# Kernel tuning notes

Hardware: AMD Instinct MI355X
Metric: run time of the kernel (lower is better)

Reference implementation:

```python
import jax, jax.numpy as jnp
import numpy as np

N_NODES = 50000
N_EDGES = 800000
IN_CH, HID_CH, OUT_CH = 128, 128, 64


def _gcn_conv(x, W, b, src, dst, n):
    """PyG GCNConv: self-loops + symmetric norm + linear + scatter-add + bias."""
    loop = jnp.arange(n, dtype=src.dtype)
    src_sl = jnp.concatenate([src, loop])  # [E+N]
    dst_sl = jnp.concatenate([dst, loop])
    # degree computed on edges incl. self-loops (edge weight 1)
    deg = jax.ops.segment_sum(jnp.ones_like(dst_sl, dtype=x.dtype), dst_sl,
                              num_segments=n)
    dinv = jnp.where(deg > 0, jax.lax.rsqrt(deg), 0.0)
    norm = dinv[src_sl] * dinv[dst_sl]  # [E+N]
    xw = x @ W  # [N, F_out]
    msg = xw[src_sl] * norm[:, None]  # gather + scale, [E+N, F_out]
    out = jax.ops.segment_sum(msg, dst_sl, num_segments=n)
    return out + b


def setup_inputs() -> dict:
    key = jax.random.key(0)
    ks = jax.random.split(key, 5)
    x = jax.random.normal(ks[0], (N_NODES, IN_CH), dtype=jnp.float32)
    edge_index = jax.random.randint(ks[1], (2, N_EDGES), 0, N_NODES, dtype=jnp.int64)
    s1 = 1.0 / np.sqrt(IN_CH)
    s2 = 1.0 / np.sqrt(HID_CH)
    W1 = jax.random.normal(ks[2], (IN_CH, HID_CH), dtype=jnp.float32) * s1
    W2 = jax.random.normal(ks[3], (HID_CH, HID_CH), dtype=jnp.float32) * s2
    W3 = jax.random.normal(ks[4], (HID_CH, OUT_CH), dtype=jnp.float32) * s2
    return {
        "x": x, "edge_index": edge_index,
        "W1": W1, "b1": jnp.zeros((HID_CH,), jnp.float32),
        "W2": W2, "b2": jnp.zeros((HID_CH,), jnp.float32),
        "W3": W3, "b3": jnp.zeros((OUT_CH,), jnp.float32),
    }


def reference(x, edge_index, W1, b1, W2, b2, W3, b3):
    n = x.shape[0]
    src, dst = edge_index[0], edge_index[1]
    # dropout(p=0.6) is identity in eval mode
    h = jax.nn.relu(_gcn_conv(x, W1, b1, src, dst, n))
    h = jax.nn.relu(_gcn_conv(h, W2, b2, src, dst, n))
    out = _gcn_conv(h, W3, b3, src, dst, n)
    return out
```

## Files before the change

### kernel.cpp

```cpp
#include <hip/hip_runtime.h>
#include <cstdint>

#define CAP 32768
#define CHUNK 2048

typedef __attribute__((ext_vector_type(8))) short bf8_t;
typedef __attribute__((ext_vector_type(4))) float f4_t;

__device__ __forceinline__ uint32_t f_to_bf(float f) {
    union { float f; uint32_t u; } v; v.f = f;
    uint32_t u = v.u;
    return (u + 0x7fffu + ((u >> 16) & 1u)) >> 16;
}
__device__ __forceinline__ float bf_to_f(uint32_t h) {
    union { uint32_t u; float f; } v; v.u = h << 16; return v.f;
}
__device__ __forceinline__ float2 bf2_to_f2(uint32_t u) {
    union { uint32_t u; float f; } a, b;
    a.u = u << 16; b.u = u & 0xffff0000u;
    float2 r; r.x = a.f; r.y = b.f; return r;
}
__device__ __forceinline__ void fma8(float* acc, uint4 u, float d) {
    float2 p0 = bf2_to_f2(u.x), p1 = bf2_to_f2(u.y);
    float2 p2 = bf2_to_f2(u.z), p3 = bf2_to_f2(u.w);
    acc[0] += p0.x * d; acc[1] += p0.y * d;
    acc[2] += p1.x * d; acc[3] += p1.y * d;
    acc[4] += p2.x * d; acc[5] += p2.y * d;
    acc[6] += p3.x * d; acc[7] += p3.y * d;
}

__device__ __forceinline__ int detect64(const int* __restrict__ e32) {
    return (e32[1] | e32[3] | e32[5] | e32[7]) == 0;
}
__device__ __forceinline__ int edge_at(const void* edges, int is64, int idx) {
    if (is64) return (int)((const long long*)edges)[idx];
    return ((const int*)edges)[idx];
}

__global__ __launch_bounds__(256) void prep_kernel(
    const float* __restrict__ W1, const float* __restrict__ W2,
    const float* __restrict__ W3,
    uint16_t* w1h, uint16_t* w1l, uint16_t* w2h, uint16_t* w2l,
    uint16_t* w3h, uint16_t* w3l, int* __restrict__ bucket_cur) {
    if (blockIdx.x == 160) {
        if (threadIdx.x < 64) bucket_cur[threadIdx.x] = threadIdx.x * CAP;
        return;
    }
    int idx = blockIdx.x * 256 + threadIdx.x;
    const float* W; uint16_t* oh; uint16_t* ol; int FOUT; int e;
    if (idx < 16384)      { W = W1; oh = w1h; ol = w1l; FOUT = 128; e = idx; }
    else if (idx < 32768) { W = W2; oh = w2h; ol = w2l; FOUT = 128; e = idx - 16384; }
    else                  { W = W3; oh = w3h; ol = w3l; FOUT = 64;  e = idx - 32768; }
    int j = e & 7;
    int lane = (e >> 3) & 63;
    int rem = e >> 9;
    int NT = FOUT >> 4;
    int nt = rem % NT, kc = rem / NT;
    int k = kc * 32 + ((lane >> 4) << 3) + j;
    int c = nt * 16 + (lane & 15);
    float v = W[(size_t)k * FOUT + c];
    uint32_t h = f_to_bf(v);
    uint32_t l = f_to_bf(v - bf_to_f(h));
    oh[e] = (uint16_t)h;
    ol[e] = (uint16_t)l;
}

__device__ __forceinline__ void gemm1_body(
    const float* __restrict__ A, const uint16_t* __restrict__ Wfhi,
    const uint16_t* __restrict__ Wflo, uint16_t* __restrict__ Yout,
    int n, int cp, int tile0, int tstride, int lane) {
    constexpr int NT = 8, NTW = 2;
    int ntiles = (n + 15) >> 4;
    bf8_t wh[NTW][4], wl[NTW][4];
#pragma unroll
    for (int t = 0; t < NTW; t++) {
        int nt = cp * NTW + t;
#pragma unroll
        for (int kc = 0; kc < 4; kc++) {
            size_t b = ((size_t)(kc * NT + nt) * 64 + lane) * 8;
            wh[t][kc] = *(const bf8_t*)&Wfhi[b];
            wl[t][kc] = *(const bf8_t*)&Wflo[b];
        }
    }
    int row_in = lane & 15;
    int koff = (lane >> 4) << 3;
    int colb = lane & 15;
    int rq = (lane >> 4) << 2;
    for (int tile = tile0; tile < ntiles; tile += tstride) {
        int R = tile << 4;
        int arow = R + row_in; if (arow >= n) arow = n - 1;
        const float* ap = A + (size_t)arow * 128 + koff;
        bf8_t ah[4], al[4];
#pragma unroll
        for (int kc = 0; kc < 4; kc++) {
            float4 pv = *(const float4*)(ap + kc * 32);
            float4 qv = *(const float4*)(ap + kc * 32 + 4);
            float vv[8] = {pv.x, pv.y, pv.z, pv.w, qv.x, qv.y, qv.z, qv.w};
#pragma unroll
            for (int j = 0; j < 8; j++) {
                uint32_t h = f_to_bf(vv[j]);
                ah[kc][j] = (short)h;
                al[kc][j] = (short)f_to_bf(vv[j] - bf_to_f(h));
            }
        }
        f4_t acc[NTW];
#pragma unroll
        for (int t = 0; t < NTW; t++) acc[t] = (f4_t){0.f, 0.f, 0.f, 0.f};
#pragma unroll
        for (int kc = 0; kc < 4; kc++) {
#pragma unroll
            for (int t = 0; t < NTW; t++) {
                acc[t] = __builtin_amdgcn_mfma_f32_16x16x32_bf16(ah[kc], wh[t][kc], acc[t], 0, 0, 0);
                acc[t] = __builtin_amdgcn_mfma_f32_16x16x32_bf16(ah[kc], wl[t][kc], acc[t], 0, 0, 0);
                acc[t] = __builtin_amdgcn_mfma_f32_16x16x32_bf16(al[kc], wh[t][kc], acc[t], 0, 0, 0);
            }
        }
#pragma unroll
        for (int t = 0; t < NTW; t++) {
            int c = (cp * NTW + t) * 16 + colb;
#pragma unroll
            for (int r = 0; r < 4; r++) {
                int row = R + rq + r;
                if (row < n)
                    Yout[(size_t)row * 128 + c] = (uint16_t)f_to_bf(acc[t][r]);
            }
        }
    }
}

__global__ __launch_bounds__(256) void scatter_gemm1_kernel(
    const void* __restrict__ ei, int* __restrict__ bucket_cur,
    int2* __restrict__ buckets, int E, int sbcnt,
    const float* __restrict__ x, const uint16_t* __restrict__ w1h,
    const uint16_t* __restrict__ w1l, uint16_t* __restrict__ y1, int n) {
    int tid = threadIdx.x;
    if ((int)blockIdx.x < sbcnt) {
        __shared__ int cnt[64];
        int base = blockIdx.x * CHUNK;
        int is64 = detect64((const int*)ei);
        if (tid < 64) cnt[tid] = 0;
        __syncthreads();
        int dloc[8];
#pragma unroll
        for (int it = 0; it < 8; it++) {
            int i = base + it * 256 + tid;
            int d = (i < E) ? edge_at(ei, is64, E + i) : -1;
            dloc[it] = d;
            if (d >= 0) atomicAdd(&cnt[d >> 10], 1);
        }
        __syncthreads();
        if (tid < 64) {
            int v = cnt[tid];
            cnt[tid] = atomicAdd(&bucket_cur[tid], v);
        }
        __syncthreads();
#pragma unroll
        for (int it = 0; it < 8; it++) {
            int i = base + it * 256 + tid;
            if (dloc[it] >= 0) {
                int s = edge_at(ei, is64, i);
                int p = atomicAdd(&cnt[dloc[it] >> 10], 1);
                buckets[p] = make_int2(s, dloc[it]);
            }
        }
    } else {
        int lane = tid & 63, wid = tid >> 6;
        gemm1_body(x, w1h, w1l, y1, n, wid, blockIdx.x - sbcnt,
                   gridDim.x - sbcnt, lane);
    }
}

__global__ __launch_bounds__(512) void csr_local_kernel(
    const int2* __restrict__ buckets, const int* __restrict__ bucket_cur,
    int* __restrict__ row_ptr, int* __restrict__ bsum, float* __restrict__ dinv, int n) {
    __shared__ int cnt[1024];
    __shared__ int sb[1024];
    int b = blockIdx.x, tid = threadIdx.x;
    int base = b << 10;
    int lim = min(1024, n - base);
    if (lim <= 0) { if (tid == 0) bsum[b] = 0; return; }
    int ecnt = bucket_cur[b] - b * CAP;
    const int2* ebase = buckets + (size_t)b * CAP;
    for (int i = tid; i < 1024; i += 512) cnt[i] = 0;
    __syncthreads();
    for (int i = tid; i < ecnt; i += 512)
        atomicAdd(&cnt[ebase[i].y - base], 1);
    __syncthreads();
    for (int i = tid; i < lim; i += 512)
        dinv[base + i] = rsqrtf((float)(cnt[i] + 1));
    __syncthreads();
    int* a = cnt; int* s = sb;
    for (int st = 1; st < 1024; st <<= 1) {
        for (int i = tid; i < 1024; i += 512)
            s[i] = a[i] + ((i >= st) ? a[i - st] : 0);
        __syncthreads();
        int* t = a; a = s; s = t;
    }
    for (int i = tid; i < lim; i += 512)
        row_ptr[base + i] = (i > 0) ? a[i - 1] : 0;
    if (tid == 0) bsum[b] = a[1023];
}

__global__ __launch_bounds__(512) void fill_bucket_kernel(
    const int2* __restrict__ buckets, const int* __restrict__ bucket_cur,
    int* __restrict__ row_ptr, const int* __restrict__ bsum,
    int* __restrict__ col, int n, int nbuck) {
    __shared__ int cur[1024];
    __shared__ int s_bo;
    int b = blockIdx.x, tid = threadIdx.x;
    int base = b << 10;
    int lim = min(1024, n - base);
    if (lim <= 0) return;
    if (tid < 64) {
        int lane = tid;
        int v = (lane < nbuck) ? bsum[lane] : 0;
        int incl = v;
#pragma unroll
        for (int off = 1; off < 64; off <<= 1) {
            int t = __shfl_up(incl, off);
            if (lane >= off) incl += t;
        }
        int tot = __shfl(incl, nbuck - 1);
        int bo = (b > 0) ? __shfl(incl, b - 1) : 0;
        if (lane == 0) {
            s_bo = bo;
            if (b == nbuck - 1) row_ptr[n] = tot;
        }
    }
    __syncthreads();
    int ecnt = bucket_cur[b] - b * CAP;
    const int2* ebase = buckets + (size_t)b * CAP;
    int bo = s_bo;
    for (int i = tid; i < lim; i += 512) {
        int v = row_ptr[base + i] + bo;
        row_ptr[base + i] = v;
        cur[i] = v;
    }
    __syncthreads();
    for (int i = tid; i < ecnt; i += 512) {
        int2 e = ebase[i];
        int p = atomicAdd(&cur[e.y - base], 1);
        col[p] = e.x;
    }
}

template <int FOUT, bool SRC_SCALE>
__global__ __launch_bounds__(256) void agg_gemm_kernel(
    const uint16_t* __restrict__ Yin, const int* __restrict__ row_ptr,
    const int* __restrict__ col, const float* __restrict__ dinv,
    const float* __restrict__ bias,
    const uint16_t* __restrict__ Wfhi, const uint16_t* __restrict__ Wflo,
    uint16_t* __restrict__ Yout, int n) {
    __shared__ uint4 hs4[16 * 17];
    __shared__ uint4 ls4[16 * 17];
    int tid = threadIdx.x, wid = tid >> 6, lane = tid & 63;
    int base = blockIdx.x * 16;
    int g = lane & 15, j = lane >> 4;
    const uint4* Y4 = (const uint4*)Yin;

    float4 bb0 = *(const float4*)&bias[g * 8];
    float4 bb1 = *(const float4*)&bias[g * 8 + 4];
    float bb[8] = {bb0.x, bb0.y, bb0.z, bb0.w, bb1.x, bb1.y, bb1.z, bb1.w};

    for (int q = 0; q < 4; q++) {
        int r = wid * 4 + q, node = base + r;
        uint4 ph = (uint4){0, 0, 0, 0}, pl = (uint4){0, 0, 0, 0};
        if (node < n) {
            float di = dinv[node];
            float aA[8] = {}, aB[8] = {};
            {
                float sd = (j == 0) ? (SRC_SCALE ? di : 1.f) : 0.f;
                uint4 su = Y4[(size_t)node * 16 + g];
                fma8(aA, su, sd);
            }
            int start = row_ptr[node], end = row_ptr[node + 1];
            for (int b = start; b < end; b += 64) {
                int cnt = min(64, end - b);
                int sv = (b + lane < end) ? col[b + lane] : 0;
                for (int k = 0; k < cnt; k += 8) {
                    int iA = k + j, iB = k + 4 + j;
                    int sA = __shfl(sv, iA & 63);
                    int sB = __shfl(sv, iB & 63);
                    float dA = (iA < cnt) ? (SRC_SCALE ? dinv[sA] : 1.f) : 0.f;
                    float dB = (iB < cnt) ? (SRC_SCALE ? dinv[sB] : 1.f) : 0.f;
                    uint4 uA = Y4[(size_t)sA * 16 + g];
                    uint4 uB = Y4[(size_t)sB * 16 + g];
                    fma8(aA, uA, dA);
                    fma8(aB, uB, dB);
                }
            }
            float o[8];
#pragma unroll
            for (int t = 0; t < 8; t++) o[t] = aA[t] + aB[t];
#pragma unroll
            for (int t = 0; t < 8; t++) o[t] += __shfl_xor(o[t], 16);
#pragma unroll
            for (int t = 0; t < 8; t++) o[t] += __shfl_xor(o[t], 32);
            uint32_t hh[8];
#pragma unroll
            for (int t = 0; t < 8; t++) {
                o[t] = fmaxf(o[t] * di + bb[t], 0.f);
                hh[t] = f_to_bf(o[t]);
            }
            ph = (uint4){hh[0] | (hh[1] << 16), hh[2] | (hh[3] << 16),
                         hh[4] | (hh[5] << 16), hh[6] | (hh[7] << 16)};
            uint32_t ll[8];
#pragma unroll
            for (int t = 0; t < 8; t++) ll[t] = f_to_bf(o[t] - bf_to_f(hh[t]));
            pl = (uint4){ll[0] | (ll[1] << 16), ll[2] | (ll[3] << 16),
                         ll[4] | (ll[5] << 16), ll[6] | (ll[7] << 16)};
        }
        if (j == 0) {
            hs4[r * 17 + g] = ph;
            ls4[r * 17 + g] = pl;
        }
    }
    __syncthreads();

    const uint16_t* hs = (const uint16_t*)hs4;
    const uint16_t* ls = (const uint16_t*)ls4;
    constexpr int NT = FOUT / 16;
    constexpr int NTW = NT / 4;
    constexpr int LDW = 136;
    int cp = wid;
    bf8_t wh[NTW][4], wl[NTW][4];
#pragma unroll
    for (int t = 0; t < NTW; t++) {
        int nt = cp * NTW + t;
#pragma unroll
        for (int kc = 0; kc < 4; kc++) {
            size_t b = ((size_t)(kc * NT + nt) * 64 + lane) * 8;
            wh[t][kc] = *(const bf8_t*)&Wfhi[b];
            wl[t][kc] = *(const bf8_t*)&Wflo[b];
        }
    }
    int koff = (lane >> 4) << 3;
    int colb = lane & 15;
    int rq = (lane >> 4) << 2;
    bf8_t ah[4], al[4];
#pragma unroll
    for (int kc = 0; kc < 4; kc++) {
        ah[kc] = *(const bf8_t*)(hs + (lane & 15) * LDW + koff + kc * 32);
        al[kc] = *(const bf8_t*)(ls + (lane & 15) * LDW + koff + kc * 32);
    }
    f4_t acc[NTW];
#pragma unroll
    for (int t = 0; t < NTW; t++) acc[t] = (f4_t){0.f, 0.f, 0.f, 0.f};
#pragma unroll
    for (int kc = 0; kc < 4; kc++) {
#pragma unroll
        for (int t = 0; t < NTW; t++) {
            acc[t] = __builtin_amdgcn_mfma_f32_16x16x32_bf16(ah[kc], wh[t][kc], acc[t], 0, 0, 0);
            acc[t] = __builtin_amdgcn_mfma_f32_16x16x32_bf16(ah[kc], wl[t][kc], acc[t], 0, 0, 0);
            acc[t] = __builtin_amdgcn_mfma_f32_16x16x32_bf16(al[kc], wh[t][kc], acc[t], 0, 0, 0);
        }
    }
#pragma unroll
    for (int t = 0; t < NTW; t++) {
        int c = (cp * NTW + t) * 16 + colb;
#pragma unroll
        for (int r = 0; r < 4; r++) {
            int row = base + rq + r;
            if (row < n) {
                float v = acc[t][r] * dinv[row];
                Yout[(size_t)row * FOUT + c] = (uint16_t)f_to_bf(v);
            }
        }
    }
}

__global__ __launch_bounds__(256) void agg_final_kernel(
    const uint16_t* __restrict__ Y, const int* __restrict__ row_ptr,
    const int* __restrict__ col, const float* __restrict__ dinv,
    const float* __restrict__ bias, float* __restrict__ out, int n) {
    int w = blockIdx.x * 4 + (threadIdx.x >> 6);
    int lane = threadIdx.x & 63;
    if (w >= n) return;
    int g = lane & 7, j = lane >> 3;
    const uint4* Y4 = (const uint4*)Y;
    float4 bb0 = *(const float4*)&bias[g * 8];
    float4 bb1 = *(const float4*)&bias[g * 8 + 4];
    float bb[8] = {bb0.x, bb0.y, bb0.z, bb0.w, bb1.x, bb1.y, bb1.z, bb1.w};

    float aA[8] = {}, aB[8] = {};
    {
        uint4 su = Y4[(size_t)w * 8 + g];
        fma8(aA, su, (j == 0) ? 1.f : 0.f);
    }
    int start = row_ptr[w], end = row_ptr[w + 1];
    for (int b = start; b < end; b += 64) {
        int cnt = min(64, end - b);
        int sv = (b + lane < end) ? col[b + lane] : 0;
        for (int k = 0; k < cnt; k += 16) {
            int iA = k + j, iB = k + 8 + j;
            int sA = __shfl(sv, iA & 63);
            int sB = __shfl(sv, iB & 63);
            float dA = (iA < cnt) ? 1.f : 0.f;
            float dB = (iB < cnt) ? 1.f : 0.f;
            uint4 uA = Y4[(size_t)sA * 8 + g];
            uint4 uB = Y4[(size_t)sB * 8 + g];
            fma8(aA, uA, dA);
            fma8(aB, uB, dB);
        }
    }
    float o[8];
#pragma unroll
    for (int t = 0; t < 8; t++) o[t] = aA[t] + aB[t];
#pragma unroll
    for (int t = 0; t < 8; t++) o[t] += __shfl_xor(o[t], 8);
#pragma unroll
    for (int t = 0; t < 8; t++) o[t] += __shfl_xor(o[t], 16);
#pragma unroll
    for (int t = 0; t < 8; t++) o[t] += __shfl_xor(o[t], 32);
    float di = dinv[w];
#pragma unroll
    for (int t = 0; t < 8; t++) o[t] = o[t] * di + bb[t];
    if (j == 0) {
        float4 o0 = {o[0], o[1], o[2], o[3]};
        float4 o1 = {o[4], o[5], o[6], o[7]};
        *(float4*)&out[(size_t)w * 64 + g * 8] = o0;
        *(float4*)&out[(size_t)w * 64 + g * 8 + 4] = o1;
    }
}

extern "C" void kernel_launch(void* const* d_in, const int* in_sizes, int n_in,
                              void* d_out, int out_size, void* d_ws, size_t ws_size,
                              hipStream_t stream) {
    const float* x  = (const float*)d_in[0];
    const void*  ei = d_in[1];
    const float* W1 = (const float*)d_in[2];
    const float* b1 = (const float*)d_in[3];
    const float* W2 = (const float*)d_in[4];
    const float* b2 = (const float*)d_in[5];
    const float* W3 = (const float*)d_in[6];
    const float* b3 = (const float*)d_in[7];
    int n = in_sizes[0] / 128;
    int E = in_sizes[1] / 2;
    int nbuck = (n + 1023) >> 10;

    char* p = (char*)d_ws;
    auto carve = [&](size_t bytes) {
        char* r = p;
        p += (bytes + 255) & ~(size_t)255;
        return r;
    };
    float*    dinv       = (float*)carve((size_t)n * 4);
    int*      row_ptr    = (int*)carve((size_t)(n + 1) * 4);
    int*      bsum       = (int*)carve(64 * 4);
    int*      bucket_cur = (int*)carve(64 * 4);
    int*      col        = (int*)carve((size_t)E * 4);
    int2*     buckets    = (int2*)carve((size_t)64 * CAP * 8);
    uint16_t* y1         = (uint16_t*)carve((size_t)n * 128 * 2);
    uint16_t* y2         = (uint16_t*)carve((size_t)n * 128 * 2);
    uint16_t* y3         = (uint16_t*)carve((size_t)n * 64 * 2);
    uint16_t* w1h        = (uint16_t*)carve(128 * 128 * 2);
    uint16_t* w1l        = (uint16_t*)carve(128 * 128 * 2);
    uint16_t* w2h        = (uint16_t*)carve(128 * 128 * 2);
    uint16_t* w2l        = (uint16_t*)carve(128 * 128 * 2);
    uint16_t* w3h        = (uint16_t*)carve(128 * 64 * 2);
    uint16_t* w3l        = (uint16_t*)carve(128 * 64 * 2);

    int sbcnt = (E + CHUNK - 1) / CHUNK;
    int fb = (n + 15) / 16;

    prep_kernel<<<161, 256, 0, stream>>>(W1, W2, W3, w1h, w1l, w2h, w2l,
                                         w3h, w3l, bucket_cur);
    scatter_gemm1_kernel<<<sbcnt + 782, 256, 0, stream>>>(
        ei, bucket_cur, buckets, E, sbcnt, x, w1h, w1l, y1, n);
    csr_local_kernel<<<nbuck, 512, 0, stream>>>(buckets, bucket_cur, row_ptr, bsum, dinv, n);
    fill_bucket_kernel<<<nbuck, 512, 0, stream>>>(buckets, bucket_cur, row_ptr, bsum,
                                                  col, n, nbuck);
    agg_gemm_kernel<128, true><<<fb, 256, 0, stream>>>(
        y1, row_ptr, col, dinv, b1, w2h, w2l, y2, n);
    agg_gemm_kernel<64, false><<<fb, 256, 0, stream>>>(
        y2, row_ptr, col, dinv, b2, w3h, w3l, y3, n);
    agg_final_kernel<<<(n + 3) / 4, 256, 0, stream>>>(
        y3, row_ptr, col, dinv, b3, (float*)d_out, n);
}
```

Before: 243.0 us.

## Merge CSR build kernels and co-schedule weight prep and GEMM1 with graph stages

Restructures the launch plan: weight hi/lo splitting now runs in spare blocks of the edge-bucketing kernel, and the per-bucket count, scan and fill steps are merged into one kernel whose spare blocks run the first GEMM. Bucket counters are zeroed with a memset and used as per-bucket counts, so each block finds its offset by scanning those counts directly, which removes the separate bsum pass. This cuts kernel launches and the serial dependency chain, but the merged CSR kernel now runs each bucket with 256 threads instead of 512, and GEMM1 now waits on the scatter stage.

```diff
diff --git a/kernel.cpp b/kernel.cpp
--- a/kernel.cpp
+++ b/kernel.cpp
@@ -37,16 +37,11 @@
     return ((const int*)edges)[idx];
 }
 
-__global__ __launch_bounds__(256) void prep_kernel(
-    const float* __restrict__ W1, const float* __restrict__ W2,
+__device__ __forceinline__ void wsplit_body(
+    int idx, const float* __restrict__ W1, const float* __restrict__ W2,
     const float* __restrict__ W3,
     uint16_t* w1h, uint16_t* w1l, uint16_t* w2h, uint16_t* w2l,
-    uint16_t* w3h, uint16_t* w3l, int* __restrict__ bucket_cur) {
-    if (blockIdx.x == 160) {
-        if (threadIdx.x < 64) bucket_cur[threadIdx.x] = threadIdx.x * CAP;
-        return;
-    }
-    int idx = blockIdx.x * 256 + threadIdx.x;
+    uint16_t* w3h, uint16_t* w3l) {
     const float* W; uint16_t* oh; uint16_t* ol; int FOUT; int e;
     if (idx < 16384)      { W = W1; oh = w1h; ol = w1l; FOUT = 128; e = idx; }
     else if (idx < 32768) { W = W2; oh = w2h; ol = w2l; FOUT = 128; e = idx - 16384; }
@@ -65,6 +60,50 @@
     ol[e] = (uint16_t)l;
 }
 
+__global__ __launch_bounds__(256) void scatter_wprep_kernel(
+    const void* __restrict__ ei, int* __restrict__ bucket_cur,
+    int2* __restrict__ buckets, int E, int sbcnt,
+    const float* __restrict__ W1, const float* __restrict__ W2,
+    const float* __restrict__ W3,
+    uint16_t* w1h, uint16_t* w1l, uint16_t* w2h, uint16_t* w2l,
+    uint16_t* w3h, uint16_t* w3l) {
+    int tid = threadIdx.x;
+    if ((int)blockIdx.x >= sbcnt) {
+        int idx = (blockIdx.x - sbcnt) * 256 + tid;
+        wsplit_body(idx, W1, W2, W3, w1h, w1l, w2h, w2l, w3h, w3l);
+        return;
+    }
+    __shared__ int cnt[64];
+    int base = blockIdx.x * CHUNK;
+    int is64 = detect64((const int*)ei);
+    if (tid < 64) cnt[tid] = 0;
+    __syncthreads();
+    int dloc[8];
+#pragma unroll
+    for (int it = 0; it < 8; it++) {
+        int i = base + it * 256 + tid;
+        int d = (i < E) ? edge_at(ei, is64, E + i) : -1;
+        dloc[it] = d;
+        if (d >= 0) atomicAdd(&cnt[d >> 10], 1);
+    }
+    __syncthreads();
+    if (tid < 64) {
+        int v = cnt[tid];
+        cnt[tid] = atomicAdd(&bucket_cur[tid], v);
+    }
+    __syncthreads();
+#pragma unroll
+    for (int it = 0; it < 8; it++) {
+        int i = base + it * 256 + tid;
+        if (dloc[it] >= 0) {
+            int s = edge_at(ei, is64, i);
+            int b = dloc[it] >> 10;
+            int p = atomicAdd(&cnt[b], 1);
+            buckets[(size_t)b * CAP + p] = make_int2(s, dloc[it]);
+        }
+    }
+}
+
 __device__ __forceinline__ void gemm1_body(
     const float* __restrict__ A, const uint16_t* __restrict__ Wfhi,
     const uint16_t* __restrict__ Wflo, uint16_t* __restrict__ Yout,
@@ -128,116 +167,66 @@
     }
 }
 
-__global__ __launch_bounds__(256) void scatter_gemm1_kernel(
-    const void* __restrict__ ei, int* __restrict__ bucket_cur,
-    int2* __restrict__ buckets, int E, int sbcnt,
+__global__ __launch_bounds__(256) void csrfill_gemm1_kernel(
+    const int2* __restrict__ buckets, const int* __restrict__ bucket_cur,
+    int* __restrict__ row_ptr, int* __restrict__ col,
+    float* __restrict__ dinv, int nbuck,
     const float* __restrict__ x, const uint16_t* __restrict__ w1h,
     const uint16_t* __restrict__ w1l, uint16_t* __restrict__ y1, int n) {
     int tid = threadIdx.x;
-    if ((int)blockIdx.x < sbcnt) {
-        __shared__ int cnt[64];
-        int base = blockIdx.x * CHUNK;
-        int is64 = detect64((const int*)ei);
-        if (tid < 64) cnt[tid] = 0;
-        __syncthreads();
-        int dloc[8];
-#pragma unroll
-        for (int it = 0; it < 8; it++) {
-            int i = base + it * 256 + tid;
-            int d = (i < E) ? edge_at(ei, is64, E + i) : -1;
-            dloc[it] = d;
-            if (d >= 0) atomicAdd(&cnt[d >> 10], 1);
-        }
-        __syncthreads();
-        if (tid < 64) {
-            int v = cnt[tid];
-            cnt[tid] = atomicAdd(&bucket_cur[tid], v);
-        }
-        __syncthreads();
-#pragma unroll
-        for (int it = 0; it < 8; it++) {
-            int i = base + it * 256 + tid;
-            if (dloc[it] >= 0) {
-                int s = edge_at(ei, is64, i);
-                int p = atomicAdd(&cnt[dloc[it] >> 10], 1);
-                buckets[p] = make_int2(s, dloc[it]);
-            }
-        }
-    } else {
+    if ((int)blockIdx.x >= nbuck) {
         int lane = tid & 63, wid = tid >> 6;
-        gemm1_body(x, w1h, w1l, y1, n, wid, blockIdx.x - sbcnt,
-                   gridDim.x - sbcnt, lane);
-    }
-}
-
-__global__ __launch_bounds__(512) void csr_local_kernel(
-    const int2* __restrict__ buckets, const int* __restrict__ bucket_cur,
-    int* __restrict__ row_ptr, int* __restrict__ bsum, float* __restrict__ dinv, int n) {
+        gemm1_body(x, w1h, w1l, y1, n, wid, blockIdx.x - nbuck,
+                   gridDim.x - nbuck, lane);
+        return;
+    }
     __shared__ int cnt[1024];
     __shared__ int sb[1024];
-    int b = blockIdx.x, tid = threadIdx.x;
+    __shared__ int cur[1024];
+    __shared__ int s_bo;
+    int b = blockIdx.x;
     int base = b << 10;
     int lim = min(1024, n - base);
-    if (lim <= 0) { if (tid == 0) bsum[b] = 0; return; }
-    int ecnt = bucket_cur[b] - b * CAP;
+    if (tid < 64) {
+        int v = (tid < nbuck) ? bucket_cur[tid] : 0;
+        int incl = v;
+#pragma unroll
+        for (int off = 1; off < 64; off <<= 1) {
+            int t = __shfl_up(incl, off);
+            if (tid >= off) incl += t;
+        }
+        int tot = __shfl(incl, nbuck - 1);
+        int bo = (b > 0) ? __shfl(incl, b - 1) : 0;
+        if (tid == 0) {
+            s_bo = bo;
+            if (b == nbuck - 1) row_ptr[n] = tot;
+        }
+    }
+    int ecnt = bucket_cur[b];
     const int2* ebase = buckets + (size_t)b * CAP;
-    for (int i = tid; i < 1024; i += 512) cnt[i] = 0;
-    __syncthreads();
-    for (int i = tid; i < ecnt; i += 512)
+    for (int i = tid; i < 1024; i += 256) cnt[i] = 0;
+    __syncthreads();
+    for (int i = tid; i < ecnt; i += 256)
         atomicAdd(&cnt[ebase[i].y - base], 1);
     __syncthreads();
-    for (int i = tid; i < lim; i += 512)
+    for (int i = tid; i < lim; i += 256)
         dinv[base + i] = rsqrtf((float)(cnt[i] + 1));
     __syncthreads();
     int* a = cnt; int* s = sb;
     for (int st = 1; st < 1024; st <<= 1) {
-        for (int i = tid; i < 1024; i += 512)
+        for (int i = tid; i < 1024; i += 256)
             s[i] = a[i] + ((i >= st) ? a[i - st] : 0);
         __syncthreads();
         int* t = a; a = s; s = t;
     }
-    for (int i = tid; i < lim; i += 512)
-        row_ptr[base + i] = (i > 0) ? a[i - 1] : 0;
-    if (tid == 0) bsum[b] = a[1023];
-}
-
-__global__ __launch_bounds__(512) void fill_bucket_kernel(
-    const int2* __restrict__ buckets, const int* __restrict__ bucket_cur,
-    int* __restrict__ row_ptr, const int* __restrict__ bsum,
-    int* __restrict__ col, int n, int nbuck) {
-    __shared__ int cur[1024];
-    __shared__ int s_bo;
-    int b = blockIdx.x, tid = threadIdx.x;
-    int base = b << 10;
-    int lim = min(1024, n - base);
-    if (lim <= 0) return;
-    if (tid < 64) {
-        int lane = tid;
-        int v = (lane < nbuck) ? bsum[lane] : 0;
-        int incl = v;
-#pragma unroll
-        for (int off = 1; off < 64; off <<= 1) {
-            int t = __shfl_up(incl, off);
-            if (lane >= off) incl += t;
-        }
-        int tot = __shfl(incl, nbuck - 1);
-        int bo = (b > 0) ? __shfl(incl, b - 1) : 0;
-        if (lane == 0) {
-            s_bo = bo;
-            if (b == nbuck - 1) row_ptr[n] = tot;
-        }
-    }
-    __syncthreads();
-    int ecnt = bucket_cur[b] - b * CAP;
-    const int2* ebase = buckets + (size_t)b * CAP;
     int bo = s_bo;
-    for (int i = tid; i < lim; i += 512) {
-        int v = row_ptr[base + i] + bo;
+    for (int i = tid; i < lim; i += 256) {
+        int v = ((i > 0) ? a[i - 1] : 0) + bo;
         row_ptr[base + i] = v;
         cur[i] = v;
     }
     __syncthreads();
-    for (int i = tid; i < ecnt; i += 512) {
+    for (int i = tid; i < ecnt; i += 256) {
         int2 e = ebase[i];
         int p = atomicAdd(&cur[e.y - base], 1);
         col[p] = e.x;
@@ -446,7 +435,6 @@
     };
     float*    dinv       = (float*)carve((size_t)n * 4);
     int*      row_ptr    = (int*)carve((size_t)(n + 1) * 4);
-    int*      bsum       = (int*)carve(64 * 4);
     int*      bucket_cur = (int*)carve(64 * 4);
     int*      col        = (int*)carve((size_t)E * 4);
     int2*     buckets    = (int2*)carve((size_t)64 * CAP * 8);
@@ -463,13 +451,13 @@
     int sbcnt = (E + CHUNK - 1) / CHUNK;
     int fb = (n + 15) / 16;
 
-    prep_kernel<<<161, 256, 0, stream>>>(W1, W2, W3, w1h, w1l, w2h, w2l,
-                                         w3h, w3l, bucket_cur);
-    scatter_gemm1_kernel<<<sbcnt + 782, 256, 0, stream>>>(
-        ei, bucket_cur, buckets, E, sbcnt, x, w1h, w1l, y1, n);
-    csr_local_kernel<<<nbuck, 512, 0, stream>>>(buckets, bucket_cur, row_ptr, bsum, dinv, n);
-    fill_bucket_kernel<<<nbuck, 512, 0, stream>>>(buckets, bucket_cur, row_ptr, bsum,
-                                                  col, n, nbuck);
+    hipMemsetAsync(bucket_cur, 0, 64 * 4, stream);
+    scatter_wprep_kernel<<<sbcnt + 160, 256, 0, stream>>>(
+        ei, bucket_cur, buckets, E, sbcnt,
+        W1, W2, W3, w1h, w1l, w2h, w2l, w3h, w3l);
+    csrfill_gemm1_kernel<<<nbuck + 782, 256, 0, stream>>>(
+        buckets, bucket_cur, row_ptr, col, dinv, nbuck,
+        x, w1h, w1l, y1, n);
     agg_gemm_kernel<128, true><<<fb, 256, 0, stream>>>(
         y1, row_ptr, col, dinv, b1, w2h, w2l, y2, n);
     agg_gemm_kernel<64, false><<<fb, 256, 0, stream>>>(
```

Result: slower. 249.7 us (+2.7%).
